# Performance work log

Hardware: AMD Instinct MI355X
Metric: run time of the kernel (lower is better)

The kernel has to match this reference:

```python
import jax, jax.numpy as jnp
import numpy as np

N_NODES = 100000
N_EDGES = 600000
IN_DIM = 128
HID = 128
N_GRAPHS = 512
N_CLASSES = 10


def setup_inputs() -> dict:
    key = jax.random.key(0)
    ks = jax.random.split(key, 8)
    feats = jax.random.normal(ks[0], (N_NODES, IN_DIM), dtype=jnp.float32)
    W = jax.random.normal(ks[1], (IN_DIM, HID), dtype=jnp.float32) * 0.05
    b = jnp.zeros((HID,), dtype=jnp.float32)
    W1 = jax.random.normal(ks[2], (HID, 12), dtype=jnp.float32) * 0.05
    b1 = jnp.zeros((12,), dtype=jnp.float32)
    W2 = jax.random.normal(ks[3], (12, N_CLASSES), dtype=jnp.float32) * 0.05
    b2 = jnp.zeros((N_CLASSES,), dtype=jnp.float32)
    src = jax.random.randint(ks[4], (N_EDGES,), 0, N_NODES, dtype=jnp.int32)
    dst = jax.random.randint(ks[5], (N_EDGES,), 0, N_NODES, dtype=jnp.int32)
    graph_ids = jnp.sort(jax.random.randint(ks[6], (N_NODES,), 0, N_GRAPHS, dtype=jnp.int32))
    return {"feats": feats, "W": W, "b": b, "W1": W1, "b1": b1, "W2": W2,
            "b2": b2, "src": src, "dst": dst, "graph_ids": graph_ids}


def reference(feats, W, b, W1, b1, W2, b2, src, dst, graph_ids):
    ones_e = jnp.ones((src.shape[0],), dtype=feats.dtype)
    # DGL GraphConv norm='both': clamp degrees to >= 1
    out_deg = jnp.maximum(jax.ops.segment_sum(ones_e, src, num_segments=N_NODES), 1.0)
    in_deg = jnp.maximum(jax.ops.segment_sum(ones_e, dst, num_segments=N_NODES), 1.0)
    norm_src = out_deg ** -0.5  # [N]
    norm_dst = in_deg ** -0.5
    x = feats * norm_src[:, None]               # scale source features
    agg = jax.ops.segment_sum(x[src], dst, num_segments=N_NODES)  # gather-scatter SpMM
    h = agg * norm_dst[:, None]
    h = jnp.maximum(h @ W + b, 0.0)             # GraphConv linear + ReLU  [N, HID]
    # mean_nodes: per-graph segment mean (empty graphs -> 0, matching DGL)
    gsum = jax.ops.segment_sum(h, graph_ids, num_segments=N_GRAPHS)
    cnt = jax.ops.segment_sum(jnp.ones((N_NODES,), h.dtype), graph_ids, num_segments=N_GRAPHS)
    hg = jnp.where(cnt[:, None] > 0, gsum / jnp.maximum(cnt, 1.0)[:, None], 0.0)
    # tiny 2-layer MLP classifier
    return (hg @ W1 + b1) @ W2 + b2             # [N_GRAPHS, N_CLASSES]
```

## Files before the change

kernel.cpp:

```cpp
#include <hip/hip_runtime.h>
#include <hip/hip_fp16.h>

#define N_NODES 100000
#define N_EDGES 600000
#define DIM 128
#define N_GRAPHS 512
#define MLP_HID 12
#define N_CLASSES 10
#define NPB 16
#define SLOT_CAP 32
#define TPAD 136

#define WFRAG_BLOCKS 8
#define EDGE1_BLOCKS ((N_EDGES + 255) / 256)
#define CONV_BLOCKS 6250

typedef _Float16 half8 __attribute__((ext_vector_type(8)));
typedef float float4v __attribute__((ext_vector_type(4)));
typedef float floatx2 __attribute__((ext_vector_type(2)));

__global__ void prep1_kernel(const int* __restrict__ src, const int* __restrict__ dst,
                             int* __restrict__ out_hist, int* __restrict__ in_hist,
                             int* __restrict__ slots,
                             const float* __restrict__ W, __half* __restrict__ wfrag) {
    int bx = blockIdx.x;
    if (bx < WFRAG_BLOCKS) {
        int item = bx * 256 + threadIdx.x;
        if (item < 2048) {
            int lane = item & 63;
            int kt = (item >> 6) & 3;
            int nt = item >> 8;
            int n = nt * 16 + (lane & 15);
            int k0 = kt * 32 + (lane >> 4) * 8;
            union { int4 i4; __half h[8]; } u;
            #pragma unroll
            for (int j = 0; j < 8; ++j) u.h[j] = __float2half(W[(k0 + j) * DIM + n]);
            ((int4*)wfrag)[item] = u.i4;
        }
        return;
    }
    int i = (bx - WFRAG_BLOCKS) * 256 + threadIdx.x;
    if (i < N_EDGES) {
        int s = src[i];
        int d = dst[i];
        atomicAdd(&out_hist[s], 1);
        int tk = atomicAdd(&in_hist[d], 1);
        if (tk < SLOT_CAP) slots[d * SLOT_CAP + tk] = s;
    }
}

__global__ void prep2_kernel(const float4* __restrict__ feats4, int2* __restrict__ feats_q,
                             const int* __restrict__ out_hist) {
    int i = blockIdx.x * 256 + threadIdx.x;
    int n = i >> 4;
    float ns = rsqrtf((float)max(out_hist[n], 1));
    float4 a = feats4[2 * i];
    float4 c = feats4[2 * i + 1];
    int lo = __builtin_amdgcn_cvt_pk_fp8_f32(a.x * ns, a.y * ns, 0, false);
    lo     = __builtin_amdgcn_cvt_pk_fp8_f32(a.z * ns, a.w * ns, lo, true);
    int hi = __builtin_amdgcn_cvt_pk_fp8_f32(c.x * ns, c.y * ns, 0, false);
    hi     = __builtin_amdgcn_cvt_pk_fp8_f32(c.z * ns, c.w * ns, hi, true);
    feats_q[i] = make_int2(lo, hi);
}

__global__ __launch_bounds__(128) void fused_gemm(
        const int* __restrict__ feats_q,
        const int* __restrict__ in_hist, const int* __restrict__ slots,
        const __half* __restrict__ wfrag,
        const float* __restrict__ bvec, const int* __restrict__ gid,
        float* __restrict__ gsum, float* __restrict__ cnt) {
    __shared__ __half tile_h[NPB][TPAD];
    int t = threadIdx.x;
    int group = t >> 5;
    int lane = t & 31;
    int node0 = blockIdx.x * NPB;

    int dv = 0;
    if (lane < 16) dv = in_hist[node0 + lane];
    int deg[4]; int es[4];
    #pragma unroll
    for (int r = 0; r < 4; ++r) {
        int j = r * 4 + group;
        deg[r] = __shfl(dv, j, 32);
        es[r] = 0;
        if (lane < min(deg[r], SLOT_CAP)) es[r] = slots[(node0 + j) * SLOT_CAP + lane];
    }

    #pragma unroll
    for (int r = 0; r < 4; ++r) {
        int j = r * 4 + group;
        int m = min(deg[r], SLOT_CAP);
        float4 a4 = make_float4(0.f, 0.f, 0.f, 0.f);
        int i = 0;
        for (; i + 4 <= m; i += 4) {
            int sn0 = __shfl(es[r], i + 0, 32), sn1 = __shfl(es[r], i + 1, 32);
            int sn2 = __shfl(es[r], i + 2, 32), sn3 = __shfl(es[r], i + 3, 32);
            int q0 = feats_q[sn0 * 32 + lane];
            int q1 = feats_q[sn1 * 32 + lane];
            int q2 = feats_q[sn2 * 32 + lane];
            int q3 = feats_q[sn3 * 32 + lane];
            floatx2 p0 = __builtin_amdgcn_cvt_pk_f32_fp8(q0, false);
            floatx2 r0 = __builtin_amdgcn_cvt_pk_f32_fp8(q0, true);
            floatx2 p1 = __builtin_amdgcn_cvt_pk_f32_fp8(q1, false);
            floatx2 r1 = __builtin_amdgcn_cvt_pk_f32_fp8(q1, true);
            floatx2 p2 = __builtin_amdgcn_cvt_pk_f32_fp8(q2, false);
            floatx2 r2 = __builtin_amdgcn_cvt_pk_f32_fp8(q2, true);
            floatx2 p3 = __builtin_amdgcn_cvt_pk_f32_fp8(q3, false);
            floatx2 r3 = __builtin_amdgcn_cvt_pk_f32_fp8(q3, true);
            a4.x += p0[0] + p1[0] + p2[0] + p3[0];
            a4.y += p0[1] + p1[1] + p2[1] + p3[1];
            a4.z += r0[0] + r1[0] + r2[0] + r3[0];
            a4.w += r0[1] + r1[1] + r2[1] + r3[1];
        }
        for (; i < m; ++i) {
            int sn = __shfl(es[r], i, 32);
            int q = feats_q[sn * 32 + lane];
            floatx2 p = __builtin_amdgcn_cvt_pk_f32_fp8(q, false);
            floatx2 rr = __builtin_amdgcn_cvt_pk_f32_fp8(q, true);
            a4.x += p[0]; a4.y += p[1]; a4.z += rr[0]; a4.w += rr[1];
        }
        float nd = rsqrtf((float)max(deg[r], 1));
        union { int2 v; __half2 h2[2]; } st;
        st.h2[0] = __floats2half2_rn(a4.x * nd, a4.y * nd);
        st.h2[1] = __floats2half2_rn(a4.z * nd, a4.w * nd);
        *(int2*)&tile_h[j][lane * 4] = st.v;
    }
    __syncthreads();

    int wave = t >> 6;
    int wl = t & 63;
    int quad = wl >> 4;
    int col = wl & 15;

    half8 afrag[4];
    #pragma unroll
    for (int kt = 0; kt < 4; ++kt)
        afrag[kt] = *reinterpret_cast<const half8*>(&tile_h[col][kt * 32 + quad * 8]);

    float4v c[4];
    #pragma unroll
    for (int nt = 0; nt < 4; ++nt) { c[nt][0] = 0.f; c[nt][1] = 0.f; c[nt][2] = 0.f; c[nt][3] = 0.f; }

    #pragma unroll
    for (int nt = 0; nt < 4; ++nt) {
        int ntile = wave * 4 + nt;
        #pragma unroll
        for (int kt = 0; kt < 4; ++kt) {
            half8 bfrag = *reinterpret_cast<const half8*>(wfrag + ((size_t)(ntile * 4 + kt) * 64 + wl) * 8);
            c[nt] = __builtin_amdgcn_mfma_f32_16x16x32_f16(afrag[kt], bfrag, c[nt], 0, 0, 0);
        }
    }

    int g0 = gid[node0];
    if (gid[node0 + NPB - 1] == g0) {
        #pragma unroll
        for (int nt = 0; nt < 4; ++nt) {
            float bb = bvec[(wave * 4 + nt) * 16 + col];
            float v = 0.f;
            #pragma unroll
            for (int i2 = 0; i2 < 4; ++i2) v += fmaxf(c[nt][i2] + bb, 0.f);
            v += __shfl_xor(v, 16, 64);
            v += __shfl_xor(v, 32, 64);
            if (wl < 16) atomicAdd(&gsum[g0 * DIM + (wave * 4 + nt) * 16 + col], v);
        }
        if (t == 0) atomicAdd(&cnt[g0], (float)NPB);
    } else {
        #pragma unroll
        for (int nt = 0; nt < 4; ++nt) {
            float bb = bvec[(wave * 4 + nt) * 16 + col];
            #pragma unroll
            for (int i2 = 0; i2 < 4; ++i2) {
                int g = gid[node0 + quad * 4 + i2];
                atomicAdd(&gsum[g * DIM + (wave * 4 + nt) * 16 + col],
                          fmaxf(c[nt][i2] + bb, 0.f));
            }
        }
        if (wave == 0 && col == 0) {
            #pragma unroll
            for (int i2 = 0; i2 < 4; ++i2)
                atomicAdd(&cnt[gid[node0 + quad * 4 + i2]], 1.0f);
        }
    }
}

__global__ __launch_bounds__(128) void mlp_kernel(
        const float* __restrict__ gsum, const float* __restrict__ cnt,
        const float* __restrict__ W1, const float* __restrict__ b1,
        const float* __restrict__ W2, const float* __restrict__ b2,
        float* __restrict__ out) {
    __shared__ float s[DIM];
    __shared__ float t1[MLP_HID];
    int g = blockIdx.x;
    int t = threadIdx.x;
    float c = cnt[g];
    s[t] = (c > 0.0f) ? (gsum[g * DIM + t] / c) : 0.0f;
    __syncthreads();
    if (t < MLP_HID) {
        float a = b1[t];
        for (int k = 0; k < DIM; ++k) a = fmaf(s[k], W1[k * MLP_HID + t], a);
        t1[t] = a;
    }
    __syncthreads();
    if (t < N_CLASSES) {
        float o = b2[t];
        #pragma unroll
        for (int j = 0; j < MLP_HID; ++j) o = fmaf(t1[j], W2[j * N_CLASSES + t], o);
        out[g * N_CLASSES + t] = o;
    }
}

extern "C" void kernel_launch(void* const* d_in, const int* in_sizes, int n_in,
                              void* d_out, int out_size, void* d_ws, size_t ws_size,
                              hipStream_t stream) {
    const float* feats = (const float*)d_in[0];
    const float* W     = (const float*)d_in[1];
    const float* b     = (const float*)d_in[2];
    const float* W1    = (const float*)d_in[3];
    const float* b1    = (const float*)d_in[4];
    const float* W2    = (const float*)d_in[5];
    const float* b2    = (const float*)d_in[6];
    const int*   src   = (const int*)d_in[7];
    const int*   dst   = (const int*)d_in[8];
    const int*   gid   = (const int*)d_in[9];
    float* out = (float*)d_out;

    char* ws = (char*)d_ws;
    int*   out_hist = (int*)ws;   ws += (size_t)N_NODES * 4;
    int*   in_hist  = (int*)ws;   ws += (size_t)N_NODES * 4;
    float* gsum     = (float*)ws; ws += (size_t)N_GRAPHS * DIM * 4;
    float* cnt      = (float*)ws; ws += (size_t)N_GRAPHS * 4;
    size_t zero_bytes = (size_t)(ws - (char*)d_ws);
    ws = (char*)(((uintptr_t)ws + 255) & ~(uintptr_t)255);
    int*    slots   = (int*)ws;    ws += (size_t)N_NODES * SLOT_CAP * 4;
    int*    feats_q = (int*)ws;    ws += (size_t)N_NODES * DIM;
    __half* wfrag   = (__half*)ws; ws += (size_t)2048 * 8 * 2;

    hipMemsetAsync(d_ws, 0, zero_bytes, stream);

    prep1_kernel<<<WFRAG_BLOCKS + EDGE1_BLOCKS, 256, 0, stream>>>(
        src, dst, out_hist, in_hist, slots, W, wfrag);

    prep2_kernel<<<CONV_BLOCKS, 256, 0, stream>>>(
        (const float4*)feats, (int2*)feats_q, out_hist);

    fused_gemm<<<N_NODES / NPB, 128, 0, stream>>>(
        feats_q, in_hist, slots, wfrag, b, gid, gsum, cnt);

    mlp_kernel<<<N_GRAPHS, 128, 0, stream>>>(gsum, cnt, W1, b1, W2, b2, out);
}
```

Baseline: 215.7 us.

## Privatize histograms, slots and graph sums per XCD with workgroup-scope atomics

Reads the XCC id from a hardware register and gives each of the 8 XCDs its own copy of the degree histograms, neighbor slot lists and per-graph sum and count buffers. Atomics drop to workgroup scope so they can resolve in the local L2 instead of device-coherent memory. Consumers reduce the 8 copies: a shuffle sum in prep2, a prefix scan that merges slot lists in fused_gemm, and a loop in the MLP. This adds memset size, extra reads and shuffle work. Workgroup-scope atomics on global memory shared between blocks on the same XCD rely on L2 coherence behaviour that is not guaranteed.

```diff
diff --git a/kernel.cpp b/kernel.cpp
--- a/kernel.cpp
+++ b/kernel.cpp
@@ -8,7 +8,8 @@
 #define MLP_HID 12
 #define N_CLASSES 10
 #define NPB 16
-#define SLOT_CAP 32
+#define NXCD 8
+#define CAPX 16
 #define TPAD 136
 
 #define WFRAG_BLOCKS 8
@@ -19,8 +20,21 @@
 typedef float float4v __attribute__((ext_vector_type(4)));
 typedef float floatx2 __attribute__((ext_vector_type(2)));
 
+__device__ __forceinline__ int xcc_id() {
+    unsigned x;
+    asm volatile("s_getreg_b32 %0, hwreg(20, 0, 4)" : "=s"(x));
+    return (int)(x & (NXCD - 1));
+}
+
+__device__ __forceinline__ int atom_add_local(int* p, int v) {
+    return __hip_atomic_fetch_add(p, v, __ATOMIC_RELAXED, __HIP_MEMORY_SCOPE_WORKGROUP);
+}
+__device__ __forceinline__ void atom_add_local_f(float* p, float v) {
+    __hip_atomic_fetch_add(p, v, __ATOMIC_RELAXED, __HIP_MEMORY_SCOPE_WORKGROUP);
+}
+
 __global__ void prep1_kernel(const int* __restrict__ src, const int* __restrict__ dst,
-                             int* __restrict__ out_hist, int* __restrict__ in_hist,
+                             int* __restrict__ out_hist_x, int* __restrict__ in_hist_x,
                              int* __restrict__ slots,
                              const float* __restrict__ W, __half* __restrict__ wfrag) {
     int bx = blockIdx.x;
@@ -39,21 +53,29 @@
         }
         return;
     }
+    int xcc = xcc_id();
     int i = (bx - WFRAG_BLOCKS) * 256 + threadIdx.x;
     if (i < N_EDGES) {
         int s = src[i];
         int d = dst[i];
-        atomicAdd(&out_hist[s], 1);
-        int tk = atomicAdd(&in_hist[d], 1);
-        if (tk < SLOT_CAP) slots[d * SLOT_CAP + tk] = s;
+        atom_add_local(&out_hist_x[xcc * N_NODES + s], 1);
+        int tk = atom_add_local(&in_hist_x[xcc * N_NODES + d], 1);
+        if (tk < CAPX) slots[((size_t)d * NXCD + xcc) * CAPX + tk] = s;
     }
 }
 
 __global__ void prep2_kernel(const float4* __restrict__ feats4, int2* __restrict__ feats_q,
-                             const int* __restrict__ out_hist) {
+                             const int* __restrict__ out_hist_x) {
     int i = blockIdx.x * 256 + threadIdx.x;
     int n = i >> 4;
-    float ns = rsqrtf((float)max(out_hist[n], 1));
+    int sub = threadIdx.x & 15;
+    int v = 0;
+    if (sub < 8) v = out_hist_x[sub * N_NODES + n];
+    v += __shfl_xor(v, 1, 16);
+    v += __shfl_xor(v, 2, 16);
+    v += __shfl_xor(v, 4, 16);
+    int od = __shfl(v, 0, 16);
+    float ns = rsqrtf((float)max(od, 1));
     float4 a = feats4[2 * i];
     float4 c = feats4[2 * i + 1];
     int lo = __builtin_amdgcn_cvt_pk_fp8_f32(a.x * ns, a.y * ns, 0, false);
@@ -65,31 +87,53 @@
 
 __global__ __launch_bounds__(128) void fused_gemm(
         const int* __restrict__ feats_q,
-        const int* __restrict__ in_hist, const int* __restrict__ slots,
+        const int* __restrict__ in_hist_x, const int* __restrict__ slots,
         const __half* __restrict__ wfrag,
         const float* __restrict__ bvec, const int* __restrict__ gid,
-        float* __restrict__ gsum, float* __restrict__ cnt) {
+        float* __restrict__ gsum_x, float* __restrict__ cnt_x) {
     __shared__ __half tile_h[NPB][TPAD];
     int t = threadIdx.x;
     int group = t >> 5;
     int lane = t & 31;
     int node0 = blockIdx.x * NPB;
-
-    int dv = 0;
-    if (lane < 16) dv = in_hist[node0 + lane];
-    int deg[4]; int es[4];
+    int xcc = xcc_id();
+
+    int degt[4]; int ms[4]; int es[4];
     #pragma unroll
     for (int r = 0; r < 4; ++r) {
         int j = r * 4 + group;
-        deg[r] = __shfl(dv, j, 32);
+        int node = node0 + j;
+        int ctrue = 0;
+        if (lane < 8) ctrue = in_hist_x[lane * N_NODES + node];
+        int c = min(ctrue, CAPX);
+        int dt = ctrue;
+        dt += __shfl_xor(dt, 1, 8);
+        dt += __shfl_xor(dt, 2, 8);
+        dt += __shfl_xor(dt, 4, 8);
+        degt[r] = __shfl(dt, 0, 32);
+        int ic = c;
+        int u1 = __shfl_up(ic, 1, 8); if ((lane & 7) >= 1) ic += u1;
+        int u2 = __shfl_up(ic, 2, 8); if ((lane & 7) >= 2) ic += u2;
+        int u3 = __shfl_up(ic, 4, 8); if ((lane & 7) >= 4) ic += u3;
+        int ex = ic - c;
+        int totc = __shfl(ic, 7, 32);
+        ms[r] = min(totc, 32);
+        int pk = (ex << 16) | c;
+        int sx = 0, sidx = 0;
+        #pragma unroll
+        for (int x = 0; x < 8; ++x) {
+            int p = __shfl(pk, x, 32);
+            int ebx = p >> 16, ecx = p & 0xffff;
+            if (lane >= ebx && lane < ebx + ecx) { sx = x; sidx = lane - ebx; }
+        }
         es[r] = 0;
-        if (lane < min(deg[r], SLOT_CAP)) es[r] = slots[(node0 + j) * SLOT_CAP + lane];
+        if (lane < ms[r]) es[r] = slots[((size_t)node * NXCD + sx) * CAPX + sidx];
     }
 
     #pragma unroll
     for (int r = 0; r < 4; ++r) {
         int j = r * 4 + group;
-        int m = min(deg[r], SLOT_CAP);
+        int m = ms[r];
         float4 a4 = make_float4(0.f, 0.f, 0.f, 0.f);
         int i = 0;
         for (; i + 4 <= m; i += 4) {
@@ -119,7 +163,7 @@
             floatx2 rr = __builtin_amdgcn_cvt_pk_f32_fp8(q, true);
             a4.x += p[0]; a4.y += p[1]; a4.z += rr[0]; a4.w += rr[1];
         }
-        float nd = rsqrtf((float)max(deg[r], 1));
+        float nd = rsqrtf((float)max(degt[r], 1));
         union { int2 v; __half2 h2[2]; } st;
         st.h2[0] = __floats2half2_rn(a4.x * nd, a4.y * nd);
         st.h2[1] = __floats2half2_rn(a4.z * nd, a4.w * nd);
@@ -151,6 +195,8 @@
         }
     }
 
+    float* gsum = gsum_x + (size_t)xcc * N_GRAPHS * DIM;
+    float* cnt  = cnt_x + (size_t)xcc * N_GRAPHS;
     int g0 = gid[node0];
     if (gid[node0 + NPB - 1] == g0) {
         #pragma unroll
@@ -161,9 +207,9 @@
             for (int i2 = 0; i2 < 4; ++i2) v += fmaxf(c[nt][i2] + bb, 0.f);
             v += __shfl_xor(v, 16, 64);
             v += __shfl_xor(v, 32, 64);
-            if (wl < 16) atomicAdd(&gsum[g0 * DIM + (wave * 4 + nt) * 16 + col], v);
-        }
-        if (t == 0) atomicAdd(&cnt[g0], (float)NPB);
+            if (wl < 16) atom_add_local_f(&gsum[g0 * DIM + (wave * 4 + nt) * 16 + col], v);
+        }
+        if (t == 0) atom_add_local_f(&cnt[g0], (float)NPB);
     } else {
         #pragma unroll
         for (int nt = 0; nt < 4; ++nt) {
@@ -171,20 +217,20 @@
             #pragma unroll
             for (int i2 = 0; i2 < 4; ++i2) {
                 int g = gid[node0 + quad * 4 + i2];
-                atomicAdd(&gsum[g * DIM + (wave * 4 + nt) * 16 + col],
-                          fmaxf(c[nt][i2] + bb, 0.f));
+                atom_add_local_f(&gsum[g * DIM + (wave * 4 + nt) * 16 + col],
+                                 fmaxf(c[nt][i2] + bb, 0.f));
             }
         }
         if (wave == 0 && col == 0) {
             #pragma unroll
             for (int i2 = 0; i2 < 4; ++i2)
-                atomicAdd(&cnt[gid[node0 + quad * 4 + i2]], 1.0f);
+                atom_add_local_f(&cnt[gid[node0 + quad * 4 + i2]], 1.0f);
         }
     }
 }
 
 __global__ __launch_bounds__(128) void mlp_kernel(
-        const float* __restrict__ gsum, const float* __restrict__ cnt,
+        const float* __restrict__ gsum_x, const float* __restrict__ cnt_x,
         const float* __restrict__ W1, const float* __restrict__ b1,
         const float* __restrict__ W2, const float* __restrict__ b2,
         float* __restrict__ out) {
@@ -192,8 +238,13 @@
     __shared__ float t1[MLP_HID];
     int g = blockIdx.x;
     int t = threadIdx.x;
-    float c = cnt[g];
-    s[t] = (c > 0.0f) ? (gsum[g * DIM + t] / c) : 0.0f;
+    float c = 0.f;
+    #pragma unroll
+    for (int x = 0; x < NXCD; ++x) c += cnt_x[x * N_GRAPHS + g];
+    float sv = 0.f;
+    #pragma unroll
+    for (int x = 0; x < NXCD; ++x) sv += gsum_x[(size_t)(x * N_GRAPHS + g) * DIM + t];
+    s[t] = (c > 0.0f) ? (sv / c) : 0.0f;
     __syncthreads();
     if (t < MLP_HID) {
         float a = b1[t];
@@ -225,26 +276,26 @@
     float* out = (float*)d_out;
 
     char* ws = (char*)d_ws;
-    int*   out_hist = (int*)ws;   ws += (size_t)N_NODES * 4;
-    int*   in_hist  = (int*)ws;   ws += (size_t)N_NODES * 4;
-    float* gsum     = (float*)ws; ws += (size_t)N_GRAPHS * DIM * 4;
-    float* cnt      = (float*)ws; ws += (size_t)N_GRAPHS * 4;
+    int*   out_hist_x = (int*)ws;   ws += (size_t)NXCD * N_NODES * 4;
+    int*   in_hist_x  = (int*)ws;   ws += (size_t)NXCD * N_NODES * 4;
+    float* gsum_x     = (float*)ws; ws += (size_t)NXCD * N_GRAPHS * DIM * 4;
+    float* cnt_x      = (float*)ws; ws += (size_t)NXCD * N_GRAPHS * 4;
     size_t zero_bytes = (size_t)(ws - (char*)d_ws);
     ws = (char*)(((uintptr_t)ws + 255) & ~(uintptr_t)255);
-    int*    slots   = (int*)ws;    ws += (size_t)N_NODES * SLOT_CAP * 4;
+    int*    slots   = (int*)ws;    ws += (size_t)N_NODES * NXCD * CAPX * 4;
     int*    feats_q = (int*)ws;    ws += (size_t)N_NODES * DIM;
     __half* wfrag   = (__half*)ws; ws += (size_t)2048 * 8 * 2;
 
     hipMemsetAsync(d_ws, 0, zero_bytes, stream);
 
     prep1_kernel<<<WFRAG_BLOCKS + EDGE1_BLOCKS, 256, 0, stream>>>(
-        src, dst, out_hist, in_hist, slots, W, wfrag);
+        src, dst, out_hist_x, in_hist_x, slots, W, wfrag);
 
     prep2_kernel<<<CONV_BLOCKS, 256, 0, stream>>>(
-        (const float4*)feats, (int2*)feats_q, out_hist);
+        (const float4*)feats, (int2*)feats_q, out_hist_x);
 
     fused_gemm<<<N_NODES / NPB, 128, 0, stream>>>(
-        feats_q, in_hist, slots, wfrag, b, gid, gsum, cnt);
-
-    mlp_kernel<<<N_GRAPHS, 128, 0, stream>>>(gsum, cnt, W1, b1, W2, b2, out);
-}
+        feats_q, in_hist_x, slots, wfrag, b, gid, gsum_x, cnt_x);
+
+    mlp_kernel<<<N_GRAPHS, 128, 0, stream>>>(gsum_x, cnt_x, W1, b1, W2, b2, out);
+}
```

Measured after the change: 210.7 us. -2.3%, faster.

## Merge prep kernels, move source-norm into gather, replace pooling atomics with partials

Applied to the files above, without the earlier changes.

Merges the edge-histogram and feature-quantisation kernels into one launch. Because quantisation no longer depends on out-degree, the source normalisation moves into the gather loop as a per-edge FMA using a prefetched rsqrt of out_hist. Per-graph atomics in the GEMM epilogue are replaced by per-block partial sums, or fp16 per-node rows for blocks that span two graphs. The MLP kernel then reduces these using binary search over the sorted graph_ids. This removes a launch and contended float atomics, at the cost of a serial per-graph reduction, extra out_hist gathers, and fp8 quantisation of unscaled features.

```diff
diff --git a/kernel.cpp b/kernel.cpp
--- a/kernel.cpp
+++ b/kernel.cpp
@@ -10,19 +10,22 @@
 #define NPB 16
 #define SLOT_CAP 32
 #define TPAD 136
+#define EPT 4
 
 #define WFRAG_BLOCKS 8
-#define EDGE1_BLOCKS ((N_EDGES + 255) / 256)
+#define EDGE_BLOCKS ((N_EDGES + 256*EPT - 1) / (256*EPT))
 #define CONV_BLOCKS 6250
+#define NBLK (N_NODES / NPB)
 
 typedef _Float16 half8 __attribute__((ext_vector_type(8)));
 typedef float float4v __attribute__((ext_vector_type(4)));
 typedef float floatx2 __attribute__((ext_vector_type(2)));
 
-__global__ void prep1_kernel(const int* __restrict__ src, const int* __restrict__ dst,
-                             int* __restrict__ out_hist, int* __restrict__ in_hist,
-                             int* __restrict__ slots,
-                             const float* __restrict__ W, __half* __restrict__ wfrag) {
+__global__ void prep_kernel(const int* __restrict__ src, const int* __restrict__ dst,
+                            int* __restrict__ out_hist, int* __restrict__ in_hist,
+                            int* __restrict__ slots,
+                            const float* __restrict__ W, __half* __restrict__ wfrag,
+                            const float4* __restrict__ feats4, int2* __restrict__ feats_q) {
     int bx = blockIdx.x;
     if (bx < WFRAG_BLOCKS) {
         int item = bx * 256 + threadIdx.x;
@@ -39,36 +42,43 @@
         }
         return;
     }
-    int i = (bx - WFRAG_BLOCKS) * 256 + threadIdx.x;
-    if (i < N_EDGES) {
-        int s = src[i];
-        int d = dst[i];
-        atomicAdd(&out_hist[s], 1);
-        int tk = atomicAdd(&in_hist[d], 1);
-        if (tk < SLOT_CAP) slots[d * SLOT_CAP + tk] = s;
-    }
-}
-
-__global__ void prep2_kernel(const float4* __restrict__ feats4, int2* __restrict__ feats_q,
-                             const int* __restrict__ out_hist) {
-    int i = blockIdx.x * 256 + threadIdx.x;
-    int n = i >> 4;
-    float ns = rsqrtf((float)max(out_hist[n], 1));
+    if (bx < WFRAG_BLOCKS + EDGE_BLOCKS) {
+        int base = (bx - WFRAG_BLOCKS) * (256 * EPT) + threadIdx.x;
+        int s[EPT], d[EPT]; bool ok[EPT];
+        #pragma unroll
+        for (int e = 0; e < EPT; ++e) {
+            int i = base + e * 256;
+            ok[e] = (i < N_EDGES);
+            s[e] = ok[e] ? src[i] : 0;
+            d[e] = ok[e] ? dst[i] : 0;
+        }
+        #pragma unroll
+        for (int e = 0; e < EPT; ++e) if (ok[e]) atomicAdd(&out_hist[s[e]], 1);
+        int tk[EPT];
+        #pragma unroll
+        for (int e = 0; e < EPT; ++e) tk[e] = ok[e] ? atomicAdd(&in_hist[d[e]], 1) : SLOT_CAP;
+        #pragma unroll
+        for (int e = 0; e < EPT; ++e)
+            if (tk[e] < SLOT_CAP) slots[d[e] * SLOT_CAP + tk[e]] = s[e];
+        return;
+    }
+    int i = (bx - WFRAG_BLOCKS - EDGE_BLOCKS) * 256 + threadIdx.x;
     float4 a = feats4[2 * i];
     float4 c = feats4[2 * i + 1];
-    int lo = __builtin_amdgcn_cvt_pk_fp8_f32(a.x * ns, a.y * ns, 0, false);
-    lo     = __builtin_amdgcn_cvt_pk_fp8_f32(a.z * ns, a.w * ns, lo, true);
-    int hi = __builtin_amdgcn_cvt_pk_fp8_f32(c.x * ns, c.y * ns, 0, false);
-    hi     = __builtin_amdgcn_cvt_pk_fp8_f32(c.z * ns, c.w * ns, hi, true);
+    int lo = __builtin_amdgcn_cvt_pk_fp8_f32(a.x, a.y, 0, false);
+    lo     = __builtin_amdgcn_cvt_pk_fp8_f32(a.z, a.w, lo, true);
+    int hi = __builtin_amdgcn_cvt_pk_fp8_f32(c.x, c.y, 0, false);
+    hi     = __builtin_amdgcn_cvt_pk_fp8_f32(c.z, c.w, hi, true);
     feats_q[i] = make_int2(lo, hi);
 }
 
 __global__ __launch_bounds__(128) void fused_gemm(
         const int* __restrict__ feats_q,
-        const int* __restrict__ in_hist, const int* __restrict__ slots,
+        const int* __restrict__ in_hist, const int* __restrict__ out_hist,
+        const int* __restrict__ slots,
         const __half* __restrict__ wfrag,
         const float* __restrict__ bvec, const int* __restrict__ gid,
-        float* __restrict__ gsum, float* __restrict__ cnt) {
+        float* __restrict__ partial, __half* __restrict__ mixed_h) {
     __shared__ __half tile_h[NPB][TPAD];
     int t = threadIdx.x;
     int group = t >> 5;
@@ -77,13 +87,16 @@
 
     int dv = 0;
     if (lane < 16) dv = in_hist[node0 + lane];
-    int deg[4]; int es[4];
+    int deg[4]; int es[4]; float nsf[4];
     #pragma unroll
     for (int r = 0; r < 4; ++r) {
         int j = r * 4 + group;
         deg[r] = __shfl(dv, j, 32);
+        int m = min(deg[r], SLOT_CAP);
         es[r] = 0;
-        if (lane < min(deg[r], SLOT_CAP)) es[r] = slots[(node0 + j) * SLOT_CAP + lane];
+        if (lane < m) es[r] = slots[(node0 + j) * SLOT_CAP + lane];
+        nsf[r] = 0.f;
+        if (lane < m) nsf[r] = rsqrtf((float)max(out_hist[es[r]], 1));
     }
 
     #pragma unroll
@@ -95,6 +108,8 @@
         for (; i + 4 <= m; i += 4) {
             int sn0 = __shfl(es[r], i + 0, 32), sn1 = __shfl(es[r], i + 1, 32);
             int sn2 = __shfl(es[r], i + 2, 32), sn3 = __shfl(es[r], i + 3, 32);
+            float ns0 = __shfl(nsf[r], i + 0, 32), ns1 = __shfl(nsf[r], i + 1, 32);
+            float ns2 = __shfl(nsf[r], i + 2, 32), ns3 = __shfl(nsf[r], i + 3, 32);
             int q0 = feats_q[sn0 * 32 + lane];
             int q1 = feats_q[sn1 * 32 + lane];
             int q2 = feats_q[sn2 * 32 + lane];
@@ -107,17 +122,21 @@
             floatx2 r2 = __builtin_amdgcn_cvt_pk_f32_fp8(q2, true);
             floatx2 p3 = __builtin_amdgcn_cvt_pk_f32_fp8(q3, false);
             floatx2 r3 = __builtin_amdgcn_cvt_pk_f32_fp8(q3, true);
-            a4.x += p0[0] + p1[0] + p2[0] + p3[0];
-            a4.y += p0[1] + p1[1] + p2[1] + p3[1];
-            a4.z += r0[0] + r1[0] + r2[0] + r3[0];
-            a4.w += r0[1] + r1[1] + r2[1] + r3[1];
+            a4.x = fmaf(p0[0], ns0, fmaf(p1[0], ns1, fmaf(p2[0], ns2, fmaf(p3[0], ns3, a4.x))));
+            a4.y = fmaf(p0[1], ns0, fmaf(p1[1], ns1, fmaf(p2[1], ns2, fmaf(p3[1], ns3, a4.y))));
+            a4.z = fmaf(r0[0], ns0, fmaf(r1[0], ns1, fmaf(r2[0], ns2, fmaf(r3[0], ns3, a4.z))));
+            a4.w = fmaf(r0[1], ns0, fmaf(r1[1], ns1, fmaf(r2[1], ns2, fmaf(r3[1], ns3, a4.w))));
         }
         for (; i < m; ++i) {
             int sn = __shfl(es[r], i, 32);
+            float nsv = __shfl(nsf[r], i, 32);
             int q = feats_q[sn * 32 + lane];
             floatx2 p = __builtin_amdgcn_cvt_pk_f32_fp8(q, false);
             floatx2 rr = __builtin_amdgcn_cvt_pk_f32_fp8(q, true);
-            a4.x += p[0]; a4.y += p[1]; a4.z += rr[0]; a4.w += rr[1];
+            a4.x = fmaf(p[0], nsv, a4.x);
+            a4.y = fmaf(p[1], nsv, a4.y);
+            a4.z = fmaf(rr[0], nsv, a4.z);
+            a4.w = fmaf(rr[1], nsv, a4.w);
         }
         float nd = rsqrtf((float)max(deg[r], 1));
         union { int2 v; __half2 h2[2]; } st;
@@ -161,30 +180,29 @@
             for (int i2 = 0; i2 < 4; ++i2) v += fmaxf(c[nt][i2] + bb, 0.f);
             v += __shfl_xor(v, 16, 64);
             v += __shfl_xor(v, 32, 64);
-            if (wl < 16) atomicAdd(&gsum[g0 * DIM + (wave * 4 + nt) * 16 + col], v);
-        }
-        if (t == 0) atomicAdd(&cnt[g0], (float)NPB);
+            if (wl < 16) partial[blockIdx.x * DIM + (wave * 4 + nt) * 16 + col] = v;
+        }
     } else {
         #pragma unroll
         for (int nt = 0; nt < 4; ++nt) {
             float bb = bvec[(wave * 4 + nt) * 16 + col];
             #pragma unroll
-            for (int i2 = 0; i2 < 4; ++i2) {
-                int g = gid[node0 + quad * 4 + i2];
-                atomicAdd(&gsum[g * DIM + (wave * 4 + nt) * 16 + col],
-                          fmaxf(c[nt][i2] + bb, 0.f));
-            }
-        }
-        if (wave == 0 && col == 0) {
-            #pragma unroll
             for (int i2 = 0; i2 < 4; ++i2)
-                atomicAdd(&cnt[gid[node0 + quad * 4 + i2]], 1.0f);
-        }
-    }
+                mixed_h[(size_t)blockIdx.x * (NPB * DIM) + (quad * 4 + i2) * DIM
+                        + (wave * 4 + nt) * 16 + col] = __float2half(fmaxf(c[nt][i2] + bb, 0.f));
+        }
+    }
+}
+
+__device__ __forceinline__ int lower_bound_i(const int* __restrict__ a, int n, int v) {
+    int lo = 0, hi = n;
+    while (lo < hi) { int mid = (lo + hi) >> 1; if (a[mid] < v) lo = mid + 1; else hi = mid; }
+    return lo;
 }
 
 __global__ __launch_bounds__(128) void mlp_kernel(
-        const float* __restrict__ gsum, const float* __restrict__ cnt,
+        const float* __restrict__ partial, const __half* __restrict__ mixed_h,
+        const int* __restrict__ gid,
         const float* __restrict__ W1, const float* __restrict__ b1,
         const float* __restrict__ W2, const float* __restrict__ b2,
         float* __restrict__ out) {
@@ -192,8 +210,23 @@
     __shared__ float t1[MLP_HID];
     int g = blockIdx.x;
     int t = threadIdx.x;
-    float c = cnt[g];
-    s[t] = (c > 0.0f) ? (gsum[g * DIM + t] / c) : 0.0f;
+    int s_g = lower_bound_i(gid, N_NODES, g);
+    int e_g = lower_bound_i(gid, N_NODES, g + 1);
+    float cntf = (float)(e_g - s_g);
+    float acc = 0.f;
+    int b_lo = (s_g + NPB - 1) >> 4;
+    int b_hi = e_g >> 4;
+    if (b_lo < b_hi) {
+        for (int b = b_lo; b < b_hi; ++b) acc += partial[b * DIM + t];
+        for (int n = s_g; n < b_lo * NPB; ++n)
+            acc += __half2float(mixed_h[(size_t)(n >> 4) * (NPB * DIM) + (n & 15) * DIM + t]);
+        for (int n = b_hi * NPB; n < e_g; ++n)
+            acc += __half2float(mixed_h[(size_t)(n >> 4) * (NPB * DIM) + (n & 15) * DIM + t]);
+    } else {
+        for (int n = s_g; n < e_g; ++n)
+            acc += __half2float(mixed_h[(size_t)(n >> 4) * (NPB * DIM) + (n & 15) * DIM + t]);
+    }
+    s[t] = (cntf > 0.f) ? (acc / cntf) : 0.f;
     __syncthreads();
     if (t < MLP_HID) {
         float a = b1[t];
@@ -227,24 +260,22 @@
     char* ws = (char*)d_ws;
     int*   out_hist = (int*)ws;   ws += (size_t)N_NODES * 4;
     int*   in_hist  = (int*)ws;   ws += (size_t)N_NODES * 4;
-    float* gsum     = (float*)ws; ws += (size_t)N_GRAPHS * DIM * 4;
-    float* cnt      = (float*)ws; ws += (size_t)N_GRAPHS * 4;
     size_t zero_bytes = (size_t)(ws - (char*)d_ws);
     ws = (char*)(((uintptr_t)ws + 255) & ~(uintptr_t)255);
     int*    slots   = (int*)ws;    ws += (size_t)N_NODES * SLOT_CAP * 4;
     int*    feats_q = (int*)ws;    ws += (size_t)N_NODES * DIM;
     __half* wfrag   = (__half*)ws; ws += (size_t)2048 * 8 * 2;
+    ws = (char*)(((uintptr_t)ws + 255) & ~(uintptr_t)255);
+    float*  partial = (float*)ws;  ws += (size_t)NBLK * DIM * 4;
+    __half* mixed_h = (__half*)ws; ws += (size_t)NBLK * NPB * DIM * 2;
 
     hipMemsetAsync(d_ws, 0, zero_bytes, stream);
 
-    prep1_kernel<<<WFRAG_BLOCKS + EDGE1_BLOCKS, 256, 0, stream>>>(
-        src, dst, out_hist, in_hist, slots, W, wfrag);
-
-    prep2_kernel<<<CONV_BLOCKS, 256, 0, stream>>>(
-        (const float4*)feats, (int2*)feats_q, out_hist);
-
-    fused_gemm<<<N_NODES / NPB, 128, 0, stream>>>(
-        feats_q, in_hist, slots, wfrag, b, gid, gsum, cnt);
-
-    mlp_kernel<<<N_GRAPHS, 128, 0, stream>>>(gsum, cnt, W1, b1, W2, b2, out);
-}
+    prep_kernel<<<WFRAG_BLOCKS + EDGE_BLOCKS + CONV_BLOCKS, 256, 0, stream>>>(
+        src, dst, out_hist, in_hist, slots, W, wfrag, (const float4*)feats, (int2*)feats_q);
+
+    fused_gemm<<<NBLK, 128, 0, stream>>>(
+        feats_q, in_hist, out_hist, slots, wfrag, b, gid, partial, mixed_h);
+
+    mlp_kernel<<<N_GRAPHS, 128, 0, stream>>>(partial, mixed_h, gid, W1, b1, W2, b2, out);
+}
```

New measurement: 202.0 us. -6.4%, faster.

## Merge all stages into one persistent kernel with software grid barriers

Applied to the files above, without the earlier changes.

Replaces the four separate launches with a single persistent kernel of 1024 blocks that runs the histogram, fp8 conversion, gather+GEMM and MLP phases, separated by atomic-based grid barriers. Per-graph sums no longer use float atomics. Each tile writes a partial row sum, or per-node fp16 values when a tile spans graph boundaries, and the MLP phase reduces these using a binary search over the sorted graph ids. This removes launch gaps and atomic contention, but it relies on all 1024 blocks being co-resident to avoid deadlock. It also adds a serial per-graph reduction loop and extra workspace traffic.

```diff
diff --git a/kernel.cpp b/kernel.cpp
--- a/kernel.cpp
+++ b/kernel.cpp
@@ -10,202 +10,250 @@
 #define NPB 16
 #define SLOT_CAP 32
 #define TPAD 136
-
-#define WFRAG_BLOCKS 8
-#define EDGE1_BLOCKS ((N_EDGES + 255) / 256)
-#define CONV_BLOCKS 6250
+#define NBLK (N_NODES / NPB)
+
+#define NBLOCKS 1024
+#define NTHREADS 256
+#define GSTRIDE (NBLOCKS * NTHREADS)
+#define NUNITS (NBLOCKS * 2)
+#define FUSED_ITERS ((NBLK + NUNITS - 1) / NUNITS)
+#define CONV_ITEMS (N_NODES * 16)
 
 typedef _Float16 half8 __attribute__((ext_vector_type(8)));
 typedef float float4v __attribute__((ext_vector_type(4)));
 typedef float floatx2 __attribute__((ext_vector_type(2)));
 
-__global__ void prep1_kernel(const int* __restrict__ src, const int* __restrict__ dst,
-                             int* __restrict__ out_hist, int* __restrict__ in_hist,
-                             int* __restrict__ slots,
-                             const float* __restrict__ W, __half* __restrict__ wfrag) {
+__device__ __forceinline__ void grid_barrier(int* cnt, int* gen) {
+    __syncthreads();
+    if (threadIdx.x == 0) {
+        __threadfence();
+        int g0 = __hip_atomic_load(gen, __ATOMIC_ACQUIRE, __HIP_MEMORY_SCOPE_AGENT);
+        int old = __hip_atomic_fetch_add(cnt, 1, __ATOMIC_ACQ_REL, __HIP_MEMORY_SCOPE_AGENT);
+        if (old == NBLOCKS - 1) {
+            __hip_atomic_store(cnt, 0, __ATOMIC_RELAXED, __HIP_MEMORY_SCOPE_AGENT);
+            __hip_atomic_fetch_add(gen, 1, __ATOMIC_ACQ_REL, __HIP_MEMORY_SCOPE_AGENT);
+        } else {
+            while (__hip_atomic_load(gen, __ATOMIC_ACQUIRE, __HIP_MEMORY_SCOPE_AGENT) == g0)
+                __builtin_amdgcn_s_sleep(8);
+        }
+        __threadfence();
+    }
+    __syncthreads();
+}
+
+__device__ __forceinline__ int lower_bound_i(const int* __restrict__ a, int n, int v) {
+    int lo = 0, hi = n;
+    while (lo < hi) { int mid = (lo + hi) >> 1; if (a[mid] < v) lo = mid + 1; else hi = mid; }
+    return lo;
+}
+
+__global__ __launch_bounds__(NTHREADS, 4) void mega_kernel(
+        const int* __restrict__ src, const int* __restrict__ dst,
+        int* __restrict__ out_hist, int* __restrict__ in_hist,
+        int* __restrict__ slots,
+        const float* __restrict__ W, __half* __restrict__ wfrag,
+        const float4* __restrict__ feats4, int* __restrict__ feats_q,
+        const float* __restrict__ bvec, const int* __restrict__ gid,
+        float* __restrict__ partial, __half* __restrict__ mixed_h,
+        const float* __restrict__ W1, const float* __restrict__ b1,
+        const float* __restrict__ W2, const float* __restrict__ b2,
+        float* __restrict__ out,
+        int* __restrict__ bar_cnt, int* __restrict__ bar_gen) {
+    __shared__ __half tile_h[2][NPB][TPAD];
+    __shared__ float mlp_s[DIM];
+    __shared__ float mlp_t1[MLP_HID];
     int bx = blockIdx.x;
-    if (bx < WFRAG_BLOCKS) {
-        int item = bx * 256 + threadIdx.x;
-        if (item < 2048) {
-            int lane = item & 63;
-            int kt = (item >> 6) & 3;
-            int nt = item >> 8;
-            int n = nt * 16 + (lane & 15);
-            int k0 = kt * 32 + (lane >> 4) * 8;
-            union { int4 i4; __half h[8]; } u;
-            #pragma unroll
-            for (int j = 0; j < 8; ++j) u.h[j] = __float2half(W[(k0 + j) * DIM + n]);
-            ((int4*)wfrag)[item] = u.i4;
-        }
-        return;
-    }
-    int i = (bx - WFRAG_BLOCKS) * 256 + threadIdx.x;
-    if (i < N_EDGES) {
+    int tid = threadIdx.x;
+    int gtid = bx * NTHREADS + tid;
+
+    if (bx < 8) {
+        int item = gtid;
+        int lane = item & 63;
+        int kt = (item >> 6) & 3;
+        int nt = item >> 8;
+        int n = nt * 16 + (lane & 15);
+        int k0 = kt * 32 + (lane >> 4) * 8;
+        union { int4 i4; __half h[8]; } u;
+        #pragma unroll
+        for (int j = 0; j < 8; ++j) u.h[j] = __float2half(W[(k0 + j) * DIM + n]);
+        ((int4*)wfrag)[item] = u.i4;
+    }
+    for (int i = gtid; i < N_EDGES; i += GSTRIDE) {
         int s = src[i];
         int d = dst[i];
         atomicAdd(&out_hist[s], 1);
         int tk = atomicAdd(&in_hist[d], 1);
         if (tk < SLOT_CAP) slots[d * SLOT_CAP + tk] = s;
     }
-}
-
-__global__ void prep2_kernel(const float4* __restrict__ feats4, int2* __restrict__ feats_q,
-                             const int* __restrict__ out_hist) {
-    int i = blockIdx.x * 256 + threadIdx.x;
-    int n = i >> 4;
-    float ns = rsqrtf((float)max(out_hist[n], 1));
-    float4 a = feats4[2 * i];
-    float4 c = feats4[2 * i + 1];
-    int lo = __builtin_amdgcn_cvt_pk_fp8_f32(a.x * ns, a.y * ns, 0, false);
-    lo     = __builtin_amdgcn_cvt_pk_fp8_f32(a.z * ns, a.w * ns, lo, true);
-    int hi = __builtin_amdgcn_cvt_pk_fp8_f32(c.x * ns, c.y * ns, 0, false);
-    hi     = __builtin_amdgcn_cvt_pk_fp8_f32(c.z * ns, c.w * ns, hi, true);
-    feats_q[i] = make_int2(lo, hi);
-}
-
-__global__ __launch_bounds__(128) void fused_gemm(
-        const int* __restrict__ feats_q,
-        const int* __restrict__ in_hist, const int* __restrict__ slots,
-        const __half* __restrict__ wfrag,
-        const float* __restrict__ bvec, const int* __restrict__ gid,
-        float* __restrict__ gsum, float* __restrict__ cnt) {
-    __shared__ __half tile_h[NPB][TPAD];
-    int t = threadIdx.x;
-    int group = t >> 5;
-    int lane = t & 31;
-    int node0 = blockIdx.x * NPB;
-
-    int dv = 0;
-    if (lane < 16) dv = in_hist[node0 + lane];
-    int deg[4]; int es[4];
-    #pragma unroll
-    for (int r = 0; r < 4; ++r) {
-        int j = r * 4 + group;
-        deg[r] = __shfl(dv, j, 32);
-        es[r] = 0;
-        if (lane < min(deg[r], SLOT_CAP)) es[r] = slots[(node0 + j) * SLOT_CAP + lane];
-    }
-
-    #pragma unroll
-    for (int r = 0; r < 4; ++r) {
-        int j = r * 4 + group;
-        int m = min(deg[r], SLOT_CAP);
-        float4 a4 = make_float4(0.f, 0.f, 0.f, 0.f);
-        int i = 0;
-        for (; i + 4 <= m; i += 4) {
-            int sn0 = __shfl(es[r], i + 0, 32), sn1 = __shfl(es[r], i + 1, 32);
-            int sn2 = __shfl(es[r], i + 2, 32), sn3 = __shfl(es[r], i + 3, 32);
-            int q0 = feats_q[sn0 * 32 + lane];
-            int q1 = feats_q[sn1 * 32 + lane];
-            int q2 = feats_q[sn2 * 32 + lane];
-            int q3 = feats_q[sn3 * 32 + lane];
-            floatx2 p0 = __builtin_amdgcn_cvt_pk_f32_fp8(q0, false);
-            floatx2 r0 = __builtin_amdgcn_cvt_pk_f32_fp8(q0, true);
-            floatx2 p1 = __builtin_amdgcn_cvt_pk_f32_fp8(q1, false);
-            floatx2 r1 = __builtin_amdgcn_cvt_pk_f32_fp8(q1, true);
-            floatx2 p2 = __builtin_amdgcn_cvt_pk_f32_fp8(q2, false);
-            floatx2 r2 = __builtin_amdgcn_cvt_pk_f32_fp8(q2, true);
-            floatx2 p3 = __builtin_amdgcn_cvt_pk_f32_fp8(q3, false);
-            floatx2 r3 = __builtin_amdgcn_cvt_pk_f32_fp8(q3, true);
-            a4.x += p0[0] + p1[0] + p2[0] + p3[0];
-            a4.y += p0[1] + p1[1] + p2[1] + p3[1];
-            a4.z += r0[0] + r1[0] + r2[0] + r3[0];
-            a4.w += r0[1] + r1[1] + r2[1] + r3[1];
-        }
-        for (; i < m; ++i) {
-            int sn = __shfl(es[r], i, 32);
-            int q = feats_q[sn * 32 + lane];
-            floatx2 p = __builtin_amdgcn_cvt_pk_f32_fp8(q, false);
-            floatx2 rr = __builtin_amdgcn_cvt_pk_f32_fp8(q, true);
-            a4.x += p[0]; a4.y += p[1]; a4.z += rr[0]; a4.w += rr[1];
-        }
-        float nd = rsqrtf((float)max(deg[r], 1));
-        union { int2 v; __half2 h2[2]; } st;
-        st.h2[0] = __floats2half2_rn(a4.x * nd, a4.y * nd);
-        st.h2[1] = __floats2half2_rn(a4.z * nd, a4.w * nd);
-        *(int2*)&tile_h[j][lane * 4] = st.v;
-    }
-    __syncthreads();
-
-    int wave = t >> 6;
-    int wl = t & 63;
-    int quad = wl >> 4;
-    int col = wl & 15;
-
-    half8 afrag[4];
-    #pragma unroll
-    for (int kt = 0; kt < 4; ++kt)
-        afrag[kt] = *reinterpret_cast<const half8*>(&tile_h[col][kt * 32 + quad * 8]);
-
-    float4v c[4];
-    #pragma unroll
-    for (int nt = 0; nt < 4; ++nt) { c[nt][0] = 0.f; c[nt][1] = 0.f; c[nt][2] = 0.f; c[nt][3] = 0.f; }
-
-    #pragma unroll
-    for (int nt = 0; nt < 4; ++nt) {
-        int ntile = wave * 4 + nt;
-        #pragma unroll
-        for (int kt = 0; kt < 4; ++kt) {
-            half8 bfrag = *reinterpret_cast<const half8*>(wfrag + ((size_t)(ntile * 4 + kt) * 64 + wl) * 8);
-            c[nt] = __builtin_amdgcn_mfma_f32_16x16x32_f16(afrag[kt], bfrag, c[nt], 0, 0, 0);
-        }
-    }
-
-    int g0 = gid[node0];
-    if (gid[node0 + NPB - 1] == g0) {
-        #pragma unroll
-        for (int nt = 0; nt < 4; ++nt) {
-            float bb = bvec[(wave * 4 + nt) * 16 + col];
-            float v = 0.f;
+    grid_barrier(bar_cnt, bar_gen);
+
+    for (int i = gtid; i < CONV_ITEMS; i += GSTRIDE) {
+        int n = i >> 4;
+        float ns = rsqrtf((float)max(out_hist[n], 1));
+        float4 a = feats4[2 * i];
+        float4 c = feats4[2 * i + 1];
+        int lo = __builtin_amdgcn_cvt_pk_fp8_f32(a.x * ns, a.y * ns, 0, false);
+        lo     = __builtin_amdgcn_cvt_pk_fp8_f32(a.z * ns, a.w * ns, lo, true);
+        int hi = __builtin_amdgcn_cvt_pk_fp8_f32(c.x * ns, c.y * ns, 0, false);
+        hi     = __builtin_amdgcn_cvt_pk_fp8_f32(c.z * ns, c.w * ns, hi, true);
+        ((int2*)feats_q)[i] = make_int2(lo, hi);
+    }
+    grid_barrier(bar_cnt, bar_gen);
+
+    {
+        int u = tid >> 7;
+        int t = tid & 127;
+        int group = t >> 5;
+        int lane = t & 31;
+        int wave = t >> 6;
+        int wl = t & 63;
+        int quad = wl >> 4;
+        int col = wl & 15;
+        const int unit = bx * 2 + u;
+
+        for (int it = 0; it < FUSED_ITERS; ++it) {
+            int tile = unit + it * NUNITS;
+            bool act = (tile < NBLK);
+            int node0 = tile * NPB;
+
+            int dv = 0;
+            if (act && lane < 16) dv = in_hist[node0 + lane];
+            int deg[4]; int es[4];
             #pragma unroll
-            for (int i2 = 0; i2 < 4; ++i2) v += fmaxf(c[nt][i2] + bb, 0.f);
-            v += __shfl_xor(v, 16, 64);
-            v += __shfl_xor(v, 32, 64);
-            if (wl < 16) atomicAdd(&gsum[g0 * DIM + (wave * 4 + nt) * 16 + col], v);
-        }
-        if (t == 0) atomicAdd(&cnt[g0], (float)NPB);
-    } else {
-        #pragma unroll
-        for (int nt = 0; nt < 4; ++nt) {
-            float bb = bvec[(wave * 4 + nt) * 16 + col];
+            for (int r = 0; r < 4; ++r) {
+                int j = r * 4 + group;
+                deg[r] = __shfl(dv, j, 32);
+                int m = min(deg[r], SLOT_CAP);
+                es[r] = 0;
+                if (act && lane < m) es[r] = slots[(node0 + j) * SLOT_CAP + lane];
+            }
+
+            if (act) {
+                #pragma unroll
+                for (int r = 0; r < 4; ++r) {
+                    int j = r * 4 + group;
+                    int m = min(deg[r], SLOT_CAP);
+                    float4 a4 = make_float4(0.f, 0.f, 0.f, 0.f);
+                    int i = 0;
+                    for (; i + 4 <= m; i += 4) {
+                        int sn0 = __shfl(es[r], i + 0, 32), sn1 = __shfl(es[r], i + 1, 32);
+                        int sn2 = __shfl(es[r], i + 2, 32), sn3 = __shfl(es[r], i + 3, 32);
+                        int q0 = feats_q[sn0 * 32 + lane];
+                        int q1 = feats_q[sn1 * 32 + lane];
+                        int q2 = feats_q[sn2 * 32 + lane];
+                        int q3 = feats_q[sn3 * 32 + lane];
+                        floatx2 p0 = __builtin_amdgcn_cvt_pk_f32_fp8(q0, false);
+                        floatx2 r0 = __builtin_amdgcn_cvt_pk_f32_fp8(q0, true);
+                        floatx2 p1 = __builtin_amdgcn_cvt_pk_f32_fp8(q1, false);
+                        floatx2 r1 = __builtin_amdgcn_cvt_pk_f32_fp8(q1, true);
+                        floatx2 p2 = __builtin_amdgcn_cvt_pk_f32_fp8(q2, false);
+                        floatx2 r2 = __builtin_amdgcn_cvt_pk_f32_fp8(q2, true);
+                        floatx2 p3 = __builtin_amdgcn_cvt_pk_f32_fp8(q3, false);
+                        floatx2 r3 = __builtin_amdgcn_cvt_pk_f32_fp8(q3, true);
+                        a4.x += p0[0] + p1[0] + p2[0] + p3[0];
+                        a4.y += p0[1] + p1[1] + p2[1] + p3[1];
+                        a4.z += r0[0] + r1[0] + r2[0] + r3[0];
+                        a4.w += r0[1] + r1[1] + r2[1] + r3[1];
+                    }
+                    for (; i < m; ++i) {
+                        int sn = __shfl(es[r], i, 32);
+                        int q = feats_q[sn * 32 + lane];
+                        floatx2 p = __builtin_amdgcn_cvt_pk_f32_fp8(q, false);
+                        floatx2 rr = __builtin_amdgcn_cvt_pk_f32_fp8(q, true);
+                        a4.x += p[0]; a4.y += p[1]; a4.z += rr[0]; a4.w += rr[1];
+                    }
+                    float nd = rsqrtf((float)max(deg[r], 1));
+                    union { int2 v; __half2 h2[2]; } st;
+                    st.h2[0] = __floats2half2_rn(a4.x * nd, a4.y * nd);
+                    st.h2[1] = __floats2half2_rn(a4.z * nd, a4.w * nd);
+                    *(int2*)&tile_h[u][j][lane * 4] = st.v;
+                }
+            }
+            __syncthreads();
+
+            if (act) {
+                half8 afrag[4];
+                #pragma unroll
+                for (int kt = 0; kt < 4; ++kt)
+                    afrag[kt] = *reinterpret_cast<const half8*>(&tile_h[u][col][kt * 32 + quad * 8]);
+
+                float4v c[4];
+                #pragma unroll
+                for (int nt = 0; nt < 4; ++nt) { c[nt][0] = 0.f; c[nt][1] = 0.f; c[nt][2] = 0.f; c[nt][3] = 0.f; }
+
+                #pragma unroll
+                for (int nt = 0; nt < 4; ++nt) {
+                    int ntile = wave * 4 + nt;
+                    #pragma unroll
+                    for (int kt = 0; kt < 4; ++kt) {
+                        half8 bfrag = *reinterpret_cast<const half8*>(wfrag + ((size_t)(ntile * 4 + kt) * 64 + wl) * 8);
+                        c[nt] = __builtin_amdgcn_mfma_f32_16x16x32_f16(afrag[kt], bfrag, c[nt], 0, 0, 0);
+                    }
+                }
+
+                int g0 = gid[node0];
+                if (gid[node0 + NPB - 1] == g0) {
+                    #pragma unroll
+                    for (int nt = 0; nt < 4; ++nt) {
+                        float bb = bvec[(wave * 4 + nt) * 16 + col];
+                        float v = 0.f;
+                        #pragma unroll
+                        for (int i2 = 0; i2 < 4; ++i2) v += fmaxf(c[nt][i2] + bb, 0.f);
+                        v += __shfl_xor(v, 16, 64);
+                        v += __shfl_xor(v, 32, 64);
+                        if (wl < 16) partial[tile * DIM + (wave * 4 + nt) * 16 + col] = v;
+                    }
+                } else {
+                    #pragma unroll
+                    for (int nt = 0; nt < 4; ++nt) {
+                        float bb = bvec[(wave * 4 + nt) * 16 + col];
+                        #pragma unroll
+                        for (int i2 = 0; i2 < 4; ++i2)
+                            mixed_h[(size_t)tile * (NPB * DIM) + (quad * 4 + i2) * DIM
+                                    + (wave * 4 + nt) * 16 + col] = __float2half(fmaxf(c[nt][i2] + bb, 0.f));
+                    }
+                }
+            }
+            __syncthreads();
+        }
+    }
+    grid_barrier(bar_cnt, bar_gen);
+
+    if (bx < N_GRAPHS) {
+        int g = bx;
+        int t = tid;
+        int s_g = lower_bound_i(gid, N_NODES, g);
+        int e_g = lower_bound_i(gid, N_NODES, g + 1);
+        float cntf = (float)(e_g - s_g);
+        if (t < DIM) {
+            float acc = 0.f;
+            int b_lo = (s_g + NPB - 1) >> 4;
+            int b_hi = e_g >> 4;
+            if (b_lo < b_hi) {
+                for (int b2_ = b_lo; b2_ < b_hi; ++b2_) acc += partial[b2_ * DIM + t];
+                for (int n = s_g; n < b_lo * NPB; ++n)
+                    acc += __half2float(mixed_h[(size_t)(n >> 4) * (NPB * DIM) + (n & 15) * DIM + t]);
+                for (int n = b_hi * NPB; n < e_g; ++n)
+                    acc += __half2float(mixed_h[(size_t)(n >> 4) * (NPB * DIM) + (n & 15) * DIM + t]);
+            } else {
+                for (int n = s_g; n < e_g; ++n)
+                    acc += __half2float(mixed_h[(size_t)(n >> 4) * (NPB * DIM) + (n & 15) * DIM + t]);
+            }
+            mlp_s[t] = (cntf > 0.f) ? (acc / cntf) : 0.f;
+        }
+        __syncthreads();
+        if (t < MLP_HID) {
+            float a = b1[t];
+            for (int k = 0; k < DIM; ++k) a = fmaf(mlp_s[k], W1[k * MLP_HID + t], a);
+            mlp_t1[t] = a;
+        }
+        __syncthreads();
+        if (t < N_CLASSES) {
+            float o = b2[t];
             #pragma unroll
-            for (int i2 = 0; i2 < 4; ++i2) {
-                int g = gid[node0 + quad * 4 + i2];
-                atomicAdd(&gsum[g * DIM + (wave * 4 + nt) * 16 + col],
-                          fmaxf(c[nt][i2] + bb, 0.f));
-            }
-        }
-        if (wave == 0 && col == 0) {
-            #pragma unroll
-            for (int i2 = 0; i2 < 4; ++i2)
-                atomicAdd(&cnt[gid[node0 + quad * 4 + i2]], 1.0f);
-        }
-    }
-}
-
-__global__ __launch_bounds__(128) void mlp_kernel(
-        const float* __restrict__ gsum, const float* __restrict__ cnt,
-        const float* __restrict__ W1, const float* __restrict__ b1,
-        const float* __restrict__ W2, const float* __restrict__ b2,
-        float* __restrict__ out) {
-    __shared__ float s[DIM];
-    __shared__ float t1[MLP_HID];
-    int g = blockIdx.x;
-    int t = threadIdx.x;
-    float c = cnt[g];
-    s[t] = (c > 0.0f) ? (gsum[g * DIM + t] / c) : 0.0f;
-    __syncthreads();
-    if (t < MLP_HID) {
-        float a = b1[t];
-        for (int k = 0; k < DIM; ++k) a = fmaf(s[k], W1[k * MLP_HID + t], a);
-        t1[t] = a;
-    }
-    __syncthreads();
-    if (t < N_CLASSES) {
-        float o = b2[t];
-        #pragma unroll
-        for (int j = 0; j < MLP_HID; ++j) o = fmaf(t1[j], W2[j * N_CLASSES + t], o);
-        out[g * N_CLASSES + t] = o;
+            for (int j = 0; j < MLP_HID; ++j) o = fmaf(mlp_t1[j], W2[j * N_CLASSES + t], o);
+            out[g * N_CLASSES + t] = o;
+        }
     }
 }
 
@@ -225,26 +273,22 @@
     float* out = (float*)d_out;
 
     char* ws = (char*)d_ws;
+    int*   bar      = (int*)ws;   ws += 256;
     int*   out_hist = (int*)ws;   ws += (size_t)N_NODES * 4;
     int*   in_hist  = (int*)ws;   ws += (size_t)N_NODES * 4;
-    float* gsum     = (float*)ws; ws += (size_t)N_GRAPHS * DIM * 4;
-    float* cnt      = (float*)ws; ws += (size_t)N_GRAPHS * 4;
     size_t zero_bytes = (size_t)(ws - (char*)d_ws);
     ws = (char*)(((uintptr_t)ws + 255) & ~(uintptr_t)255);
     int*    slots   = (int*)ws;    ws += (size_t)N_NODES * SLOT_CAP * 4;
     int*    feats_q = (int*)ws;    ws += (size_t)N_NODES * DIM;
     __half* wfrag   = (__half*)ws; ws += (size_t)2048 * 8 * 2;
+    ws = (char*)(((uintptr_t)ws + 255) & ~(uintptr_t)255);
+    float*  partial = (float*)ws;  ws += (size_t)NBLK * DIM * 4;
+    __half* mixed_h = (__half*)ws; ws += (size_t)NBLK * NPB * DIM * 2;
 
     hipMemsetAsync(d_ws, 0, zero_bytes, stream);
 
-    prep1_kernel<<<WFRAG_BLOCKS + EDGE1_BLOCKS, 256, 0, stream>>>(
-        src, dst, out_hist, in_hist, slots, W, wfrag);
-
-    prep2_kernel<<<CONV_BLOCKS, 256, 0, stream>>>(
-        (const float4*)feats, (int2*)feats_q, out_hist);
-
-    fused_gemm<<<N_NODES / NPB, 128, 0, stream>>>(
-        feats_q, in_hist, slots, wfrag, b, gid, gsum, cnt);
-
-    mlp_kernel<<<N_GRAPHS, 128, 0, stream>>>(gsum, cnt, W1, b1, W2, b2, out);
-}
+    mega_kernel<<<NBLOCKS, NTHREADS, 0, stream>>>(
+        src, dst, out_hist, in_hist, slots, W, wfrag,
+        (const float4*)feats, feats_q, b, gid, partial, mixed_h,
+        W1, b1, W2, b2, out, bar, bar + 1);
+}
```

New measurement: 847.1 us. +292.8%, slower.
